# Kernel tuning notes

Hardware: AMD Instinct MI355X
Metric: run time of the kernel (lower is better)

The kernel has to match this reference:

```python
import jax, jax.numpy as jnp
import numpy as np
import math

N_HEADS = 16

def setup_inputs() -> dict:
    key = jax.random.key(0)
    ks = jax.random.split(key, 5)
    B, S, D = 4, 2048, 1024
    scale = 0.02
    return {
        "x": jax.random.normal(ks[0], (B, S, D), dtype=jnp.float32),
        "w_in": jax.random.normal(ks[1], (D, 3 * D), dtype=jnp.float32) * scale,
        "b_in": jax.random.normal(ks[2], (3 * D,), dtype=jnp.float32) * scale,
        "w_out": jax.random.normal(ks[3], (D, D), dtype=jnp.float32) * scale,
        "b_out": jax.random.normal(ks[4], (D,), dtype=jnp.float32) * scale,
    }

def reference(x, w_in, b_in, w_out, b_out):
    B, S, D = x.shape
    H = N_HEADS
    dh = D // H
    qkv = x @ w_in + b_in                      # [B,S,3D]
    q, k, v = jnp.split(qkv, 3, axis=-1)
    # [B,S,D] -> [B,H,S,dh]
    q = q.reshape(B, S, H, dh).transpose(0, 2, 1, 3)
    k = k.reshape(B, S, H, dh).transpose(0, 2, 1, 3)
    v = v.reshape(B, S, H, dh).transpose(0, 2, 1, 3)
    scores = jnp.einsum("bhqd,bhkd->bhqk", q, k) / math.sqrt(dh)
    causal = jnp.tril(jnp.ones((S, S), dtype=bool))  # allow k <= q
    scores = jnp.where(causal, scores, -jnp.inf)
    wei = jax.nn.softmax(scores, axis=-1)
    out = jnp.einsum("bhqk,bhkd->bhqd", wei, v)      # [B,H,S,dh]
    out = out.transpose(0, 2, 1, 3).reshape(B, S, D)
    return out @ w_out + b_out
```

## Files before the change

kernel.cpp:

```cpp
#include <hip/hip_runtime.h>

typedef unsigned short u16;
typedef unsigned int   u32;
typedef float  f32x4  __attribute__((ext_vector_type(4)));
typedef __bf16 bf16x8 __attribute__((ext_vector_type(8)));
typedef unsigned short u16x8 __attribute__((ext_vector_type(8)));

__device__ __forceinline__ u16 f2bf(float f) {
  u32 u = __builtin_bit_cast(u32, f);
  u = (u + 0x7fffu + ((u >> 16) & 1u)) >> 16;
  return (u16)u;
}

__device__ __forceinline__ void gload_lds16(const void* g, void* l) {
  __builtin_amdgcn_global_load_lds(
      (const __attribute__((address_space(1))) void*)g,
      (__attribute__((address_space(3))) void*)l, 16, 0, 0);
}

__global__ __launch_bounds__(256) void conv_f32_bf16(
    const float* __restrict__ in, u16* __restrict__ out, int n8) {
  int i = blockIdx.x * 256 + threadIdx.x;
  if (i >= n8) return;
  const float4* p = (const float4*)in;
  float4 a = p[2 * i], b = p[2 * i + 1];
  u16x8 r;
  r[0] = f2bf(a.x); r[1] = f2bf(a.y); r[2] = f2bf(a.z); r[3] = f2bf(a.w);
  r[4] = f2bf(b.x); r[5] = f2bf(b.y); r[6] = f2bf(b.z); r[7] = f2bf(b.w);
  ((u16x8*)out)[i] = r;
}

__global__ __launch_bounds__(256) void conv_transpose(
    const float* __restrict__ in, u16* __restrict__ out, int K, int N) {
  __shared__ float tile[64][65];
  int nb = N >> 6;
  int tk = blockIdx.x / nb, tn = blockIdx.x % nb;
  int t = threadIdx.x;
  int kl = t >> 4, n4 = (t & 15) * 4;
#pragma unroll
  for (int i = 0; i < 4; ++i) {
    int k = kl + 16 * i;
    float4 v = *(const float4*)(in + (size_t)(tk * 64 + k) * N + tn * 64 + n4);
    tile[k][n4] = v.x; tile[k][n4 + 1] = v.y; tile[k][n4 + 2] = v.z; tile[k][n4 + 3] = v.w;
  }
  __syncthreads();
  int nl = t >> 4, k4 = (t & 15) * 4;
#pragma unroll
  for (int i = 0; i < 4; ++i) {
    int n = nl + 16 * i;
    ushort4 o;
    o.x = f2bf(tile[k4 + 0][n]); o.y = f2bf(tile[k4 + 1][n]);
    o.z = f2bf(tile[k4 + 2][n]); o.w = f2bf(tile[k4 + 3][n]);
    *(ushort4*)(out + (size_t)(tn * 64 + n) * K + tk * 64 + k4) = o;
  }
}

template <int OUT_BF16>
__global__ __launch_bounds__(256, 2) void gemm_kernel(
    const u16* __restrict__ A, const u16* __restrict__ Bt,
    const float* __restrict__ bias, void* __restrict__ C,
    int M, int N, int K) {
  __shared__ __align__(16) char smem[32768];
  char* As = smem;
  char* Bs = smem + 16384;
  int tid = threadIdx.x, w = tid >> 6, lane = tid & 63;
  int g = lane >> 4, l15 = lane & 15, l7 = lane & 7;
  int nblk = N >> 7;
  int bm = blockIdx.x / nblk, bn = blockIdx.x % nblk;
  int m0 = bm << 7, n0 = bn << 7;
  int wm = w >> 1, wn = w & 1;

  f32x4 acc[4][4];
#pragma unroll
  for (int i = 0; i < 4; ++i)
#pragma unroll
    for (int j = 0; j < 4; ++j) acc[i][j] = f32x4{0.f, 0.f, 0.f, 0.f};

  int kiter = K >> 6;
  for (int kt = 0; kt < kiter; ++kt) {
    __syncthreads();
#pragma unroll
    for (int i = 0; i < 4; ++i) {
      int rbase = 32 * w + 8 * i;
      int row = rbase + (lane >> 3);
      int koff = kt * 64 + 8 * (l7 ^ (row & 7));
      gload_lds16(A + (size_t)(m0 + row) * K + koff, As + rbase * 128);
      gload_lds16(Bt + (size_t)(n0 + row) * K + koff, Bs + rbase * 128);
    }
    __syncthreads();
#pragma unroll
    for (int ks = 0; ks < 2; ++ks) {
      bf16x8 af[4], bf[4];
#pragma unroll
      for (int mi = 0; mi < 4; ++mi) {
        int ml = wm * 64 + mi * 16 + l15;
        af[mi] = *(const bf16x8*)(As + ml * 128 + ((ks * 64 + g * 16) ^ ((ml & 7) << 4)));
      }
#pragma unroll
      for (int ni = 0; ni < 4; ++ni) {
        int nl = wn * 64 + ni * 16 + l15;
        bf[ni] = *(const bf16x8*)(Bs + nl * 128 + ((ks * 64 + g * 16) ^ ((nl & 7) << 4)));
      }
#pragma unroll
      for (int mi = 0; mi < 4; ++mi)
#pragma unroll
        for (int ni = 0; ni < 4; ++ni)
          acc[mi][ni] = __builtin_amdgcn_mfma_f32_16x16x32_bf16(af[mi], bf[ni], acc[mi][ni], 0, 0, 0);
    }
  }

#pragma unroll
  for (int ni = 0; ni < 4; ++ni) {
    int col = n0 + wn * 64 + ni * 16 + l15;
    float bv = bias[col];
#pragma unroll
    for (int mi = 0; mi < 4; ++mi) {
      int rowb = m0 + wm * 64 + mi * 16 + g * 4;
#pragma unroll
      for (int r = 0; r < 4; ++r) {
        float v = acc[mi][ni][r] + bv;
        if (OUT_BF16)
          ((u16*)C)[(size_t)(rowb + r) * N + col] = f2bf(v);
        else
          ((float*)C)[(size_t)(rowb + r) * N + col] = v;
      }
    }
  }
}

__global__ __launch_bounds__(256, 2) void attn_fwd(
    const u16* __restrict__ qkv, u16* __restrict__ aout) {
  const int S = 2048, D3 = 3072;
  int bh = blockIdx.x & 63;
  int qt = 31 - (blockIdx.x >> 6);
  int b = bh >> 4, h = bh & 15;
  const u16* qb = qkv + (size_t)b * S * D3;

  int tid = threadIdx.x;
  int w = tid >> 6, lane = tid & 63;
  int g = lane >> 4, l15 = lane & 15, l7 = lane & 7;

  __shared__ __align__(16) char Kb[8192];
  __shared__ __align__(16) char Vb[8192];
  __shared__ __align__(16) char Pb[8192];

  int qrow = qt * 64 + w * 16 + l15;
  const u16* qp = qb + (size_t)qrow * D3 + h * 64 + g * 8;
  bf16x8 qf0 = *(const bf16x8*)qp;
  bf16x8 qf1 = *(const bf16x8*)(qp + 32);

  f32x4 o_acc[4];
#pragma unroll
  for (int i = 0; i < 4; ++i) o_acc[i] = f32x4{0.f, 0.f, 0.f, 0.f};
  float m_r[4] = {-3e38f, -3e38f, -3e38f, -3e38f};
  float l_r[4] = {0.f, 0.f, 0.f, 0.f};

  char* pw = Pb + w * 2048;

  for (int kvt = 0; kvt <= qt; ++kvt) {
    __syncthreads();
#pragma unroll
    for (int i = 0; i < 2; ++i) {
      int rbase = w * 16 + i * 8;
      int row = rbase + (lane >> 3);
      const u16* src = qb + (size_t)(kvt * 64 + row) * D3 + 1024 + h * 64 + 8 * (l7 ^ (row & 7));
      gload_lds16(src, Kb + rbase * 128);
    }
    {
      int kv0 = w * 16 + ((lane >> 3) << 1);
      int d0 = l7 * 8;
      const u16* vs = qb + (size_t)(kvt * 64 + kv0) * D3 + 2048 + h * 64 + d0;
      u16x8 v0 = *(const u16x8*)vs;
      u16x8 v1 = *(const u16x8*)(vs + D3);
#pragma unroll
      for (int j = 0; j < 8; ++j) {
        int d = d0 + j;
        u32 val = (u32)v0[j] | ((u32)v1[j] << 16);
        int sw = ((d & 7) ^ (d >> 3)) << 4;
        *(u32*)(Vb + d * 128 + ((2 * kv0) ^ sw)) = val;
      }
    }
    __syncthreads();

    f32x4 s_acc[4];
#pragma unroll
    for (int nb = 0; nb < 4; ++nb) {
      int kv = nb * 16 + l15;
      const char* kb = Kb + kv * 128;
      int sw = (kv & 7) << 4;
      bf16x8 kf0 = *(const bf16x8*)(kb + ((g * 16) ^ sw));
      bf16x8 kf1 = *(const bf16x8*)(kb + ((64 + g * 16) ^ sw));
      f32x4 z = {0.f, 0.f, 0.f, 0.f};
      z = __builtin_amdgcn_mfma_f32_16x16x32_bf16(qf0, kf0, z, 0, 0, 0);
      z = __builtin_amdgcn_mfma_f32_16x16x32_bf16(qf1, kf1, z, 0, 0, 0);
      s_acc[nb] = z;
    }

    bool diag = (kvt == qt);
#pragma unroll
    for (int r = 0; r < 4; ++r) {
      int qloc = w * 16 + g * 4 + r;
#pragma unroll
      for (int nb = 0; nb < 4; ++nb) {
        float s = s_acc[nb][r] * 0.125f;
        if (diag && (nb * 16 + l15) > qloc) s = -1e30f;
        s_acc[nb][r] = s;
      }
      float pm = fmaxf(fmaxf(s_acc[0][r], s_acc[1][r]), fmaxf(s_acc[2][r], s_acc[3][r]));
      pm = fmaxf(pm, __shfl_xor(pm, 1));
      pm = fmaxf(pm, __shfl_xor(pm, 2));
      pm = fmaxf(pm, __shfl_xor(pm, 4));
      pm = fmaxf(pm, __shfl_xor(pm, 8));
      float newm = fmaxf(m_r[r], pm);
      float corr = __expf(m_r[r] - newm);
      float rs = 0.f;
#pragma unroll
      for (int nb = 0; nb < 4; ++nb) {
        float p = __expf(s_acc[nb][r] - newm);
        s_acc[nb][r] = p;
        rs += p;
      }
      rs += __shfl_xor(rs, 1);
      rs += __shfl_xor(rs, 2);
      rs += __shfl_xor(rs, 4);
      rs += __shfl_xor(rs, 8);
      l_r[r] = l_r[r] * corr + rs;
      m_r[r] = newm;
#pragma unroll
      for (int nb = 0; nb < 4; ++nb) o_acc[nb][r] *= corr;
    }

#pragma unroll
    for (int r = 0; r < 4; ++r) {
      int q = g * 4 + r;
      int sw = (q & 7) << 4;
#pragma unroll
      for (int nb = 0; nb < 4; ++nb) {
        int kv = nb * 16 + l15;
        *(u16*)(pw + q * 128 + ((2 * kv) ^ sw)) = f2bf(s_acc[nb][r]);
      }
    }
    __syncthreads();

#pragma unroll
    for (int ks = 0; ks < 2; ++ks) {
      bf16x8 pf = *(const bf16x8*)(pw + l15 * 128 + ((ks * 64 + g * 16) ^ ((l15 & 7) << 4)));
#pragma unroll
      for (int nb = 0; nb < 4; ++nb) {
        int d = nb * 16 + l15;
        int sw = ((d & 7) ^ (d >> 3)) << 4;
        bf16x8 vf = *(const bf16x8*)(Vb + d * 128 + ((ks * 64 + g * 16) ^ sw));
        o_acc[nb] = __builtin_amdgcn_mfma_f32_16x16x32_bf16(pf, vf, o_acc[nb], 0, 0, 0);
      }
    }
  }

#pragma unroll
  for (int nb = 0; nb < 4; ++nb) {
    int col = h * 64 + nb * 16 + l15;
#pragma unroll
    for (int r = 0; r < 4; ++r) {
      int row = b * S + qt * 64 + w * 16 + g * 4 + r;
      aout[(size_t)row * 1024 + col] = f2bf(o_acc[nb][r] / l_r[r]);
    }
  }
}

extern "C" void kernel_launch(void* const* d_in, const int* in_sizes, int n_in,
                              void* d_out, int out_size, void* d_ws, size_t ws_size,
                              hipStream_t stream) {
  (void)in_sizes; (void)n_in; (void)out_size;
  const float* x     = (const float*)d_in[0];
  const float* w_in  = (const float*)d_in[1];
  const float* b_in  = (const float*)d_in[2];
  const float* w_out = (const float*)d_in[3];
  const float* b_out = (const float*)d_in[4];
  float* out = (float*)d_out;
  char* ws = (char*)d_ws;
  if (ws_size < 92274688u) return;

  u16* xb     = (u16*)(ws);
  u16* w_inT  = (u16*)(ws + (16u << 20));
  u16* w_outT = (u16*)(ws + (22u << 20));
  u16* qkv    = (u16*)(ws + (24u << 20));
  u16* aout   = (u16*)(ws + (72u << 20));

  conv_f32_bf16<<<4096, 256, 0, stream>>>(x, xb, 1048576);
  conv_transpose<<<768, 256, 0, stream>>>(w_in, w_inT, 1024, 3072);
  conv_transpose<<<256, 256, 0, stream>>>(w_out, w_outT, 1024, 1024);
  gemm_kernel<1><<<1536, 256, 0, stream>>>(xb, w_inT, b_in, qkv, 8192, 3072, 1024);
  attn_fwd<<<2048, 256, 0, stream>>>(qkv, aout);
  gemm_kernel<0><<<512, 256, 0, stream>>>(aout, w_outT, b_out, out, 8192, 1024, 1024);
}
```

Baseline: 298.1 us.

## Double-buffer K/V tiles and keep P in registers via transposed MFMA

The attention kernel now double-buffers the K and V tiles in shared memory, prefetching the next tile while the current one is computed, so each iteration has one barrier instead of three. It computes S transposed (K·Q) so each lane owns one query row, which turns the softmax reductions into cross-group shuffles and lets the probabilities feed the PV MFMA straight from registers through the 16x16x16 bf16 instruction, with no LDS round trip for P. Output stores are vectorised and MFMA sections are wrapped in setprio. The cost is twice the LDS for K/V, extra registers for the prefetched V, and a fallback shuffle path if the 16x16x16 builtin is missing.

```diff
diff --git a/kernel.cpp b/kernel.cpp
--- a/kernel.cpp
+++ b/kernel.cpp
@@ -4,7 +4,10 @@
 typedef unsigned int   u32;
 typedef float  f32x4  __attribute__((ext_vector_type(4)));
 typedef __bf16 bf16x8 __attribute__((ext_vector_type(8)));
+typedef __bf16 bf16x4 __attribute__((ext_vector_type(4)));
+typedef short  s16x4  __attribute__((ext_vector_type(4)));
 typedef unsigned short u16x8 __attribute__((ext_vector_type(8)));
+typedef unsigned int   u32x4 __attribute__((ext_vector_type(4)));
 
 __device__ __forceinline__ u16 f2bf(float f) {
   u32 u = __builtin_bit_cast(u32, f);
@@ -128,6 +131,46 @@
   }
 }
 
+
+#if __has_builtin(__builtin_amdgcn_mfma_f32_16x16x16bf16_1k)
+#define HAVE_MFMA16 1
+__device__ __forceinline__ f32x4 mfma16(s16x4 a, s16x4 b, f32x4 c) {
+  return __builtin_amdgcn_mfma_f32_16x16x16bf16_1k(a, b, c, 0, 0, 0);
+}
+#endif
+
+struct V2reg { u16x8 a, b; };
+
+__device__ __forceinline__ void stage_k(const u16* qb, char* kbuf, int kvt,
+                                        int h, int w, int lane) {
+  int l7 = lane & 7;
+#pragma unroll
+  for (int i = 0; i < 2; ++i) {
+    int rbase = w * 16 + i * 8;
+    int row = rbase + (lane >> 3);
+    const u16* src = qb + (size_t)(kvt * 64 + row) * 3072 + 1024 + h * 64 + 8 * (l7 ^ (row & 7));
+    gload_lds16(src, kbuf + rbase * 128);
+  }
+}
+
+__device__ __forceinline__ V2reg load_v(const u16* qb, int kvt, int h, int kv0, int d0) {
+  const u16* vs = qb + (size_t)(kvt * 64 + kv0) * 3072 + 2048 + h * 64 + d0;
+  V2reg r;
+  r.a = *(const u16x8*)vs;
+  r.b = *(const u16x8*)(vs + 3072);
+  return r;
+}
+
+__device__ __forceinline__ void write_v(char* vbuf, V2reg v, int kv0, int d0) {
+#pragma unroll
+  for (int j = 0; j < 8; ++j) {
+    int d = d0 + j;
+    u32 val = (u32)v.a[j] | ((u32)v.b[j] << 16);
+    int sw = ((d & 7) ^ (d >> 3)) << 4;
+    *(u32*)(vbuf + d * 128 + ((2 * kv0) ^ sw)) = val;
+  }
+}
+
 __global__ __launch_bounds__(256, 2) void attn_fwd(
     const u16* __restrict__ qkv, u16* __restrict__ aout) {
   const int S = 2048, D3 = 3072;
@@ -140,129 +183,162 @@
   int w = tid >> 6, lane = tid & 63;
   int g = lane >> 4, l15 = lane & 15, l7 = lane & 7;
 
-  __shared__ __align__(16) char Kb[8192];
-  __shared__ __align__(16) char Vb[8192];
-  __shared__ __align__(16) char Pb[8192];
+  __shared__ __align__(16) char Kb[2][8192];
+  __shared__ __align__(16) char Vb[2][8192];
 
   int qrow = qt * 64 + w * 16 + l15;
   const u16* qp = qb + (size_t)qrow * D3 + h * 64 + g * 8;
   bf16x8 qf0 = *(const bf16x8*)qp;
   bf16x8 qf1 = *(const bf16x8*)(qp + 32);
 
-  f32x4 o_acc[4];
-#pragma unroll
-  for (int i = 0; i < 4; ++i) o_acc[i] = f32x4{0.f, 0.f, 0.f, 0.f};
-  float m_r[4] = {-3e38f, -3e38f, -3e38f, -3e38f};
-  float l_r[4] = {0.f, 0.f, 0.f, 0.f};
-
-  char* pw = Pb + w * 2048;
-
+  f32x4 oaT[4];
+#pragma unroll
+  for (int i = 0; i < 4; ++i) oaT[i] = f32x4{0.f, 0.f, 0.f, 0.f};
+  float m_s = -3e38f, l_s = 0.f;
+
+  int vkv0 = w * 16 + ((lane >> 3) << 1);
+  int vd0 = l7 * 8;
+
+  stage_k(qb, Kb[0], 0, h, w, lane);
+  {
+    V2reg v = load_v(qb, 0, h, vkv0, vd0);
+    write_v(Vb[0], v, vkv0, vd0);
+  }
+  __syncthreads();
+
+  V2reg vreg;
   for (int kvt = 0; kvt <= qt; ++kvt) {
-    __syncthreads();
-#pragma unroll
-    for (int i = 0; i < 2; ++i) {
-      int rbase = w * 16 + i * 8;
-      int row = rbase + (lane >> 3);
-      const u16* src = qb + (size_t)(kvt * 64 + row) * D3 + 1024 + h * 64 + 8 * (l7 ^ (row & 7));
-      gload_lds16(src, Kb + rbase * 128);
-    }
-    {
-      int kv0 = w * 16 + ((lane >> 3) << 1);
-      int d0 = l7 * 8;
-      const u16* vs = qb + (size_t)(kvt * 64 + kv0) * D3 + 2048 + h * 64 + d0;
-      u16x8 v0 = *(const u16x8*)vs;
-      u16x8 v1 = *(const u16x8*)(vs + D3);
-#pragma unroll
-      for (int j = 0; j < 8; ++j) {
-        int d = d0 + j;
-        u32 val = (u32)v0[j] | ((u32)v1[j] << 16);
-        int sw = ((d & 7) ^ (d >> 3)) << 4;
-        *(u32*)(Vb + d * 128 + ((2 * kv0) ^ sw)) = val;
-      }
-    }
-    __syncthreads();
-
-    f32x4 s_acc[4];
+    int cur = kvt & 1;
+    if (kvt < qt) {
+      stage_k(qb, Kb[cur ^ 1], kvt + 1, h, w, lane);
+      vreg = load_v(qb, kvt + 1, h, vkv0, vd0);
+    }
+
+    f32x4 sT[4];
+    __builtin_amdgcn_s_setprio(1);
 #pragma unroll
     for (int nb = 0; nb < 4; ++nb) {
       int kv = nb * 16 + l15;
-      const char* kb = Kb + kv * 128;
+      const char* kb = Kb[cur] + kv * 128;
       int sw = (kv & 7) << 4;
       bf16x8 kf0 = *(const bf16x8*)(kb + ((g * 16) ^ sw));
       bf16x8 kf1 = *(const bf16x8*)(kb + ((64 + g * 16) ^ sw));
       f32x4 z = {0.f, 0.f, 0.f, 0.f};
-      z = __builtin_amdgcn_mfma_f32_16x16x32_bf16(qf0, kf0, z, 0, 0, 0);
-      z = __builtin_amdgcn_mfma_f32_16x16x32_bf16(qf1, kf1, z, 0, 0, 0);
-      s_acc[nb] = z;
-    }
-
-    bool diag = (kvt == qt);
-#pragma unroll
-    for (int r = 0; r < 4; ++r) {
-      int qloc = w * 16 + g * 4 + r;
+      z = __builtin_amdgcn_mfma_f32_16x16x32_bf16(kf0, qf0, z, 0, 0, 0);
+      z = __builtin_amdgcn_mfma_f32_16x16x32_bf16(kf1, qf1, z, 0, 0, 0);
+      sT[nb] = z;
+    }
+    __builtin_amdgcn_s_setprio(0);
+
+#pragma unroll
+    for (int nb = 0; nb < 4; ++nb)
+#pragma unroll
+      for (int r = 0; r < 4; ++r) sT[nb][r] *= 0.125f;
+    if (kvt == qt) {
+      int qloc = w * 16 + l15;
+#pragma unroll
+      for (int nb = 0; nb < 4; ++nb)
+#pragma unroll
+        for (int r = 0; r < 4; ++r)
+          if (nb * 16 + g * 4 + r > qloc) sT[nb][r] = -1e30f;
+    }
+
+    float pm = -3e38f;
+#pragma unroll
+    for (int nb = 0; nb < 4; ++nb)
+#pragma unroll
+      for (int r = 0; r < 4; ++r) pm = fmaxf(pm, sT[nb][r]);
+    pm = fmaxf(pm, __shfl_xor(pm, 16));
+    pm = fmaxf(pm, __shfl_xor(pm, 32));
+    float newm = fmaxf(m_s, pm);
+    float corr = __expf(m_s - newm);
+    float rs = 0.f;
+#pragma unroll
+    for (int nb = 0; nb < 4; ++nb)
+#pragma unroll
+      for (int r = 0; r < 4; ++r) {
+        float e = __expf(sT[nb][r] - newm);
+        sT[nb][r] = e;
+        rs += e;
+      }
+    rs += __shfl_xor(rs, 16);
+    rs += __shfl_xor(rs, 32);
+    l_s = l_s * corr + rs;
+    m_s = newm;
+#pragma unroll
+    for (int db = 0; db < 4; ++db)
+#pragma unroll
+      for (int r = 0; r < 4; ++r) oaT[db][r] *= corr;
+
+#ifdef HAVE_MFMA16
+    s16x4 pf[4];
+#pragma unroll
+    for (int nb = 0; nb < 4; ++nb) {
+      bf16x4 t;
+#pragma unroll
+      for (int r = 0; r < 4; ++r) t[r] = (__bf16)sT[nb][r];
+      pf[nb] = __builtin_bit_cast(s16x4, t);
+    }
+    __builtin_amdgcn_s_setprio(1);
+#pragma unroll
+    for (int db = 0; db < 4; ++db) {
+      int d = db * 16 + l15;
+      const char* vb = Vb[cur] + d * 128;
+      int swd = ((d & 7) ^ (d >> 3)) << 4;
 #pragma unroll
       for (int nb = 0; nb < 4; ++nb) {
-        float s = s_acc[nb][r] * 0.125f;
-        if (diag && (nb * 16 + l15) > qloc) s = -1e30f;
-        s_acc[nb][r] = s;
-      }
-      float pm = fmaxf(fmaxf(s_acc[0][r], s_acc[1][r]), fmaxf(s_acc[2][r], s_acc[3][r]));
-      pm = fmaxf(pm, __shfl_xor(pm, 1));
-      pm = fmaxf(pm, __shfl_xor(pm, 2));
-      pm = fmaxf(pm, __shfl_xor(pm, 4));
-      pm = fmaxf(pm, __shfl_xor(pm, 8));
-      float newm = fmaxf(m_r[r], pm);
-      float corr = __expf(m_r[r] - newm);
-      float rs = 0.f;
-#pragma unroll
-      for (int nb = 0; nb < 4; ++nb) {
-        float p = __expf(s_acc[nb][r] - newm);
-        s_acc[nb][r] = p;
-        rs += p;
-      }
-      rs += __shfl_xor(rs, 1);
-      rs += __shfl_xor(rs, 2);
-      rs += __shfl_xor(rs, 4);
-      rs += __shfl_xor(rs, 8);
-      l_r[r] = l_r[r] * corr + rs;
-      m_r[r] = newm;
-#pragma unroll
-      for (int nb = 0; nb < 4; ++nb) o_acc[nb][r] *= corr;
-    }
-
-#pragma unroll
-    for (int r = 0; r < 4; ++r) {
-      int q = g * 4 + r;
-      int sw = (q & 7) << 4;
-#pragma unroll
-      for (int nb = 0; nb < 4; ++nb) {
-        int kv = nb * 16 + l15;
-        *(u16*)(pw + q * 128 + ((2 * kv) ^ sw)) = f2bf(s_acc[nb][r]);
-      }
-    }
-    __syncthreads();
-
-#pragma unroll
-    for (int ks = 0; ks < 2; ++ks) {
-      bf16x8 pf = *(const bf16x8*)(pw + l15 * 128 + ((ks * 64 + g * 16) ^ ((l15 & 7) << 4)));
-#pragma unroll
-      for (int nb = 0; nb < 4; ++nb) {
-        int d = nb * 16 + l15;
-        int sw = ((d & 7) ^ (d >> 3)) << 4;
-        bf16x8 vf = *(const bf16x8*)(Vb + d * 128 + ((ks * 64 + g * 16) ^ sw));
-        o_acc[nb] = __builtin_amdgcn_mfma_f32_16x16x32_bf16(pf, vf, o_acc[nb], 0, 0, 0);
-      }
-    }
-  }
-
-#pragma unroll
-  for (int nb = 0; nb < 4; ++nb) {
-    int col = h * 64 + nb * 16 + l15;
-#pragma unroll
-    for (int r = 0; r < 4; ++r) {
-      int row = b * S + qt * 64 + w * 16 + g * 4 + r;
-      aout[(size_t)row * 1024 + col] = f2bf(o_acc[nb][r] / l_r[r]);
-    }
+        bf16x4 vf = *(const bf16x4*)(vb + ((nb * 32 + g * 8) ^ swd));
+        oaT[db] = mfma16(__builtin_bit_cast(s16x4, vf), pf[nb], oaT[db]);
+      }
+    }
+    __builtin_amdgcn_s_setprio(0);
+#else
+    u32 wlo[4], whi[4];
+#pragma unroll
+    for (int nb = 0; nb < 4; ++nb) {
+      wlo[nb] = (u32)f2bf(sT[nb][0]) | ((u32)f2bf(sT[nb][1]) << 16);
+      whi[nb] = (u32)f2bf(sT[nb][2]) | ((u32)f2bf(sT[nb][3]) << 16);
+    }
+    int srcA = (2 * (g & 1)) * 16 + l15;
+    int srcB = srcA + 16;
+    bool hi = (g >> 1) != 0;
+    __builtin_amdgcn_s_setprio(1);
+#pragma unroll
+    for (int kb2 = 0; kb2 < 2; ++kb2) {
+      int nbE = kb2 * 2, nbO = kb2 * 2 + 1;
+      u32 a0 = __shfl(wlo[nbE], srcA), a1 = __shfl(whi[nbE], srcA);
+      u32 a2 = __shfl(wlo[nbE], srcB), a3 = __shfl(whi[nbE], srcB);
+      u32 b0 = __shfl(wlo[nbO], srcA), b1 = __shfl(whi[nbO], srcA);
+      u32 b2 = __shfl(wlo[nbO], srcB), b3 = __shfl(whi[nbO], srcB);
+      u32x4 ow = {hi ? b0 : a0, hi ? b1 : a1, hi ? b2 : a2, hi ? b3 : a3};
+      bf16x8 pfrag = __builtin_bit_cast(bf16x8, ow);
+#pragma unroll
+      for (int db = 0; db < 4; ++db) {
+        int d = db * 16 + l15;
+        int swd = ((d & 7) ^ (d >> 3)) << 4;
+        bf16x8 vf = *(const bf16x8*)(Vb[cur] + d * 128 + ((kb2 * 64 + g * 16) ^ swd));
+        oaT[db] = __builtin_amdgcn_mfma_f32_16x16x32_bf16(vf, pfrag, oaT[db], 0, 0, 0);
+      }
+    }
+    __builtin_amdgcn_s_setprio(0);
+#endif
+
+    if (kvt < qt) {
+      write_v(Vb[cur ^ 1], vreg, vkv0, vd0);
+      __syncthreads();
+    }
+  }
+
+  float inv = 1.0f / l_s;
+  size_t obase = (size_t)(b * S + qt * 64 + w * 16 + l15) * 1024 + h * 64;
+#pragma unroll
+  for (int db = 0; db < 4; ++db) {
+    ushort4 st;
+    st.x = f2bf(oaT[db][0] * inv);
+    st.y = f2bf(oaT[db][1] * inv);
+    st.z = f2bf(oaT[db][2] * inv);
+    st.w = f2bf(oaT[db][3] * inv);
+    *(ushort4*)(aout + obase + db * 16 + g * 4) = st;
   }
 }
 
```

New measurement: 261.9 us. -12.1%, faster.
